# Kernel optimization log

Measured on AMD Instinct MI355X. Metric: run time of the kernel, lower is better.

The kernel has to match this reference:

```python
import jax, jax.numpy as jnp
import numpy as np

I, H, L, O = 11, 33, 3, 18

def lstm_layer(x_tbi, W_ih, W_hh, b_ih, b_hh):
    # x_tbi: [T, B, in]; W_ih: [4H, in]; W_hh: [4H, H]
    T, B = x_tbi.shape[0], x_tbi.shape[1]
    # precompute input contribution for all timesteps (one big GEMM)
    xg = jnp.einsum('tbi,gi->tbg', x_tbi, W_ih) + b_ih + b_hh  # [T, B, 4H]
    h0 = jnp.zeros((B, H), x_tbi.dtype)
    c0 = jnp.zeros((B, H), x_tbi.dtype)

    def step(carry, xg_t):
        h, c = carry
        gates = xg_t + h @ W_hh.T                      # [B, 4H]
        i, f, g, o = jnp.split(gates, 4, axis=-1)      # PyTorch gate order i,f,g,o
        i = jax.nn.sigmoid(i)
        f = jax.nn.sigmoid(f)
        g = jnp.tanh(g)
        o = jax.nn.sigmoid(o)
        c = f * c + i * g
        h = o * jnp.tanh(c)
        return (h, c), h

    (hT, cT), ys = jax.lax.scan(step, (h0, c0), xg)
    return ys, hT, cT  # ys: [T, B, H]


def setup_inputs() -> dict:
    key = jax.random.key(0)
    ks = jax.random.split(key, 20)
    B, T = 512, 2048
    s = 1.0 / np.sqrt(H)
    d = {'x': jax.random.normal(ks[0], (B, T, I), jnp.float32)}
    in_sizes = [I, H, H]
    for l in range(L):
        d[f'W_ih{l}'] = jax.random.uniform(ks[1 + 4 * l], (4 * H, in_sizes[l]), jnp.float32, -s, s)
        d[f'W_hh{l}'] = jax.random.uniform(ks[2 + 4 * l], (4 * H, H), jnp.float32, -s, s)
        d[f'b_ih{l}'] = jax.random.uniform(ks[3 + 4 * l], (4 * H,), jnp.float32, -s, s)
        d[f'b_hh{l}'] = jax.random.uniform(ks[4 + 4 * l], (4 * H,), jnp.float32, -s, s)
    d['W1'] = jax.random.normal(ks[13], (4 * O, H), jnp.float32) * 0.05
    d['b1'] = jnp.zeros((4 * O,), jnp.float32)
    d['W2'] = jax.random.normal(ks[14], (O, 4 * O), jnp.float32) * 0.05
    d['b2'] = jnp.zeros((O,), jnp.float32)
    return d


def reference(x, W_ih0, W_hh0, b_ih0, b_hh0, W_ih1, W_hh1, b_ih1, b_hh1,
              W_ih2, W_hh2, b_ih2, b_hh2, W1, b1, W2, b2):
    # x: [B, T, I] (batch_first) -> time-major for scan
    xt = jnp.transpose(x, (1, 0, 2))  # [T, B, I]
    params = [(W_ih0, W_hh0, b_ih0, b_hh0),
              (W_ih1, W_hh1, b_ih1, b_hh1),
              (W_ih2, W_hh2, b_ih2, b_hh2)]
    hiddens = []
    cur = xt
    for (Wi, Wh, bi, bh) in params:
        cur, hT, _ = lstm_layer(cur, Wi, Wh, bi, bh)
        hiddens.append(hT)
    hidden = jnp.stack(hiddens, axis=0)  # [L, B, H] (final hidden state per layer)
    # MLP head (dropout inactive at inference); torch nn.GELU default = exact erf
    h1 = jax.nn.gelu(hidden @ W1.T + b1, approximate=False)
    out = h1 @ W2.T + b2  # [L, B, O]
    return out, hidden
```

## Files before the change

kernel.cpp:

```cpp
#include <hip/hip_runtime.h>
#include <math.h>

#define TT 2048
#define BB 512
#define II 11
#define HH 33
#define NL 3
#define OO 18
#define HSLOT 48

typedef _Float16 h2 __attribute__((ext_vector_type(2)));
typedef _Float16 h8 __attribute__((ext_vector_type(8)));

__device__ __forceinline__ float sigm_f(float x) {
    float e = __expf(-x);
    return __builtin_amdgcn_rcpf(1.0f + e);
}
__device__ __forceinline__ float tanh_f(float x) {
    float e = __expf(2.0f * x);
    return 1.0f - 2.0f * __builtin_amdgcn_rcpf(e + 1.0f);
}

__device__ __forceinline__ h8 gldh8(const float* p, int k0, int rem) {
    h8 v;
    #pragma unroll
    for (int i = 0; i < 8; ++i) v[i] = (_Float16)((k0 + i < rem) ? p[k0 + i] : 0.0f);
    return v;
}
__device__ __forceinline__ h2 gldh2(const float* p, int k0, int rem) {
    h2 v;
    v.x = (_Float16)((k0 + 0 < rem) ? p[k0 + 0] : 0.0f);
    v.y = (_Float16)((k0 + 1 < rem) ? p[k0 + 1] : 0.0f);
    return v;
}

#define D8(a, v, w) do { \
    a = __builtin_amdgcn_fdot2((v).s01, (w).s01, a, false); \
    a = __builtin_amdgcn_fdot2((v).s23, (w).s23, a, false); \
    a = __builtin_amdgcn_fdot2((v).s45, (w).s45, a, false); \
    a = __builtin_amdgcn_fdot2((v).s67, (w).s67, a, false); } while (0)
#define D1(a, v, w) a = __builtin_amdgcn_fdot2((v), (w), a, false)

__global__ __launch_bounds__(128, 1) void lstm_pipeline_kernel(
    const float* __restrict__ x,
    const float* __restrict__ Wih0, const float* __restrict__ Whh0,
    const float* __restrict__ bih0, const float* __restrict__ bhh0,
    const float* __restrict__ Wih1, const float* __restrict__ Whh1,
    const float* __restrict__ bih1, const float* __restrict__ bhh1,
    const float* __restrict__ Wih2, const float* __restrict__ Whh2,
    const float* __restrict__ bih2, const float* __restrict__ bhh2,
    float* __restrict__ hidden_out)
{
    __shared__ __align__(16) _Float16 buf[2][NL + 1][HSLOT];

    const int tid = threadIdx.x;
    const int bg  = blockIdx.x;

    for (int i = tid; i < 2 * (NL + 1) * HSLOT; i += 128)
        ((_Float16*)buf)[i] = (_Float16)0.0f;

    const bool comp = (tid < 99);
    const int  u    = tid;
    const int  l    = (u < 33) ? 0 : (u < 66) ? 1 : 2;
    const int  j    = u - 33 * l;

    const int  pi   = tid - 99;
    const bool pref = (pi >= 0) && (pi < II);
    const float* xrow = x + (size_t)bg * TT * II + (pref ? pi : 0);

    h8 z8 = {0,0,0,0,0,0,0,0};
    h2 z2 = {(_Float16)0.0f, (_Float16)0.0f};
    h8 x00=z8,x01=z8,x02=z8,x03=z8; h2 x0t=z2;
    h8 x10=z8,x11=z8,x12=z8,x13=z8; h2 x1t=z2;
    h8 x20=z8,x21=z8,x22=z8,x23=z8; h2 x2t=z2;
    h8 x30=z8,x31=z8,x32=z8,x33=z8; h2 x3t=z2;
    h8 h00=z8,h01=z8,h02=z8,h03=z8; h2 h0t=z2;
    h8 h10=z8,h11=z8,h12=z8,h13=z8; h2 h1t=z2;
    h8 h20=z8,h21=z8,h22=z8,h23=z8; h2 h2t=z2;
    h8 h30=z8,h31=z8,h32=z8,h33=z8; h2 h3t=z2;
    float b0 = 0.0f, b1 = 0.0f, b2 = 0.0f, b3 = 0.0f;

    if (comp) {
        const float* bip = (l == 0) ? bih0 : (l == 1) ? bih1 : bih2;
        const float* bhp = (l == 0) ? bhh0 : (l == 1) ? bhh1 : bhh2;
        b0 = bip[0 * HH + j] + bhp[0 * HH + j];
        b1 = bip[1 * HH + j] + bhp[1 * HH + j];
        b2 = bip[2 * HH + j] + bhp[2 * HH + j];
        b3 = bip[3 * HH + j] + bhp[3 * HH + j];

        const float* Wi = (l == 0) ? Wih0 : (l == 1) ? Wih1 : Wih2;
        const float* Wh = (l == 0) ? Whh0 : (l == 1) ? Whh1 : Whh2;
        const int kin = (l == 0) ? II : HH;
        const float* r0 = Wi + (0 * HH + j) * kin;
        const float* r1 = Wi + (1 * HH + j) * kin;
        const float* r2 = Wi + (2 * HH + j) * kin;
        const float* r3 = Wi + (3 * HH + j) * kin;
        x00=gldh8(r0,0,kin); x01=gldh8(r0,8,kin); x02=gldh8(r0,16,kin); x03=gldh8(r0,24,kin); x0t=gldh2(r0,32,kin);
        x10=gldh8(r1,0,kin); x11=gldh8(r1,8,kin); x12=gldh8(r1,16,kin); x13=gldh8(r1,24,kin); x1t=gldh2(r1,32,kin);
        x20=gldh8(r2,0,kin); x21=gldh8(r2,8,kin); x22=gldh8(r2,16,kin); x23=gldh8(r2,24,kin); x2t=gldh2(r2,32,kin);
        x30=gldh8(r3,0,kin); x31=gldh8(r3,8,kin); x32=gldh8(r3,16,kin); x33=gldh8(r3,24,kin); x3t=gldh2(r3,32,kin);
        const float* s0 = Wh + (0 * HH + j) * HH;
        const float* s1 = Wh + (1 * HH + j) * HH;
        const float* s2 = Wh + (2 * HH + j) * HH;
        const float* s3 = Wh + (3 * HH + j) * HH;
        h00=gldh8(s0,0,HH); h01=gldh8(s0,8,HH); h02=gldh8(s0,16,HH); h03=gldh8(s0,24,HH); h0t=gldh2(s0,32,HH);
        h10=gldh8(s1,0,HH); h11=gldh8(s1,8,HH); h12=gldh8(s1,16,HH); h13=gldh8(s1,24,HH); h1t=gldh2(s1,32,HH);
        h20=gldh8(s2,0,HH); h21=gldh8(s2,8,HH); h22=gldh8(s2,16,HH); h23=gldh8(s2,24,HH); h2t=gldh2(s2,32,HH);
        h30=gldh8(s3,0,HH); h31=gldh8(s3,8,HH); h32=gldh8(s3,16,HH); h33=gldh8(s3,24,HH); h3t=gldh2(s3,32,HH);
    }

    __syncthreads();
    float v_next = 0.0f, v_next2 = 0.0f;
    if (pref) {
        buf[0][0][pi] = (_Float16)xrow[0];
        v_next  = xrow[II];
        v_next2 = xrow[2 * II];
    }
    __syncthreads();

    float c = 0.0f;

    const _Float16* rin[2]  = { &buf[0][l][0],     &buf[1][l][0] };
    const _Float16* rown[2] = { &buf[0][l + 1][0], &buf[1][l + 1][0] };
    _Float16*       wrp[2]  = { &buf[0][l + 1][j], &buf[1][l + 1][j] };
    _Float16*       pxp[2]  = { &buf[0][0][pi],    &buf[1][0][pi] };

    auto step = [&](int s, int rp, bool check, bool out, bool xload, bool xstore)
        __attribute__((always_inline)) {
        const int wp = rp ^ 1;
        if (pref) {
            if (xstore) *pxp[wp] = (_Float16)v_next;
            v_next = v_next2;
            if (xload) v_next2 = xrow[(size_t)(s + 3) * II];
        }
        const bool active = check ? (comp && (s >= l) && (s - l < TT)) : comp;
        if (active) {
            const h8* VI = (const h8*)rin[rp];
            const h8 vi0 = VI[0], vi1 = VI[1], vi2 = VI[2], vi3 = VI[3];
            const h2 vit = *(const h2*)(rin[rp] + 32);
            const h8* VO = (const h8*)rown[rp];
            const h8 vo0 = VO[0], vo1 = VO[1], vo2 = VO[2], vo3 = VO[3];
            const h2 vot = *(const h2*)(rown[rp] + 32);

            float a0 = b0, a1 = b1, a2 = b2, a3 = b3;
            D8(a0, vi0, x00); D8(a1, vi0, x10); D8(a2, vi0, x20); D8(a3, vi0, x30);
            D8(a0, vi1, x01); D8(a1, vi1, x11); D8(a2, vi1, x21); D8(a3, vi1, x31);
            D8(a0, vi2, x02); D8(a1, vi2, x12); D8(a2, vi2, x22); D8(a3, vi2, x32);
            D8(a0, vi3, x03); D8(a1, vi3, x13); D8(a2, vi3, x23); D8(a3, vi3, x33);
            D1(a0, vit, x0t); D1(a1, vit, x1t); D1(a2, vit, x2t); D1(a3, vit, x3t);
            D8(a0, vo0, h00); D8(a1, vo0, h10); D8(a2, vo0, h20); D8(a3, vo0, h30);
            D8(a0, vo1, h01); D8(a1, vo1, h11); D8(a2, vo1, h21); D8(a3, vo1, h31);
            D8(a0, vo2, h02); D8(a1, vo2, h12); D8(a2, vo2, h22); D8(a3, vo2, h32);
            D8(a0, vo3, h03); D8(a1, vo3, h13); D8(a2, vo3, h23); D8(a3, vo3, h33);
            D1(a0, vot, h0t); D1(a1, vot, h1t); D1(a2, vot, h2t); D1(a3, vot, h3t);

            const float ig = sigm_f(a0);
            const float fg = sigm_f(a1);
            const float gg = tanh_f(a2);
            const float og = sigm_f(a3);
            c = __builtin_fmaf(fg, c, ig * gg);
            const float hnew = og * tanh_f(c);

            *wrp[wp] = (_Float16)hnew;
            if (out && (s - l == TT - 1))
                hidden_out[((size_t)l * BB + bg) * HH + j] = hnew;
        }
        __syncthreads();
    };

    step(0, 0, true, false, true, true);
    step(1, 1, true, false, true, true);
    for (int s = 2; s < TT - 4; s += 2) {
        step(s,     0, false, false, true, true);
        step(s + 1, 1, false, false, true, true);
    }
    step(TT - 4, 0, false, false, true,  true);
    step(TT - 3, 1, false, false, false, true);
    step(TT - 2, 0, false, false, false, true);
    step(TT - 1, 1, false, true,  false, false);
    step(TT,     0, true,  true,  false, false);
    step(TT + 1, 1, true,  true,  false, false);
}

__global__ void mlp_head_kernel(const float* __restrict__ hidden,
                                const float* __restrict__ W1, const float* __restrict__ b1,
                                const float* __restrict__ W2, const float* __restrict__ b2,
                                float* __restrict__ out)
{
    const int row = blockIdx.x * blockDim.x + threadIdx.x;
    if (row >= NL * BB) return;

    float hv[HH];
    #pragma unroll
    for (int k = 0; k < HH; ++k) hv[k] = hidden[row * HH + k];

    float h1[4 * OO];
    #pragma unroll
    for (int m = 0; m < 4 * OO; ++m) {
        float a = b1[m];
        #pragma unroll
        for (int k = 0; k < HH; ++k) a += hv[k] * W1[m * HH + k];
        h1[m] = 0.5f * a * (1.0f + erff(a * 0.70710678118654752f));
    }
    #pragma unroll
    for (int o = 0; o < OO; ++o) {
        float a = b2[o];
        #pragma unroll
        for (int m = 0; m < 4 * OO; ++m) a += h1[m] * W2[o * (4 * OO) + m];
        out[row * OO + o] = a;
    }
}

extern "C" void kernel_launch(void* const* d_in, const int* in_sizes, int n_in,
                              void* d_out, int out_size, void* d_ws, size_t ws_size,
                              hipStream_t stream) {
    const float* x    = (const float*)d_in[0];
    const float* Wih0 = (const float*)d_in[1];
    const float* Whh0 = (const float*)d_in[2];
    const float* bih0 = (const float*)d_in[3];
    const float* bhh0 = (const float*)d_in[4];
    const float* Wih1 = (const float*)d_in[5];
    const float* Whh1 = (const float*)d_in[6];
    const float* bih1 = (const float*)d_in[7];
    const float* bhh1 = (const float*)d_in[8];
    const float* Wih2 = (const float*)d_in[9];
    const float* Whh2 = (const float*)d_in[10];
    const float* bih2 = (const float*)d_in[11];
    const float* bhh2 = (const float*)d_in[12];
    const float* W1   = (const float*)d_in[13];
    const float* b1   = (const float*)d_in[14];
    const float* W2   = (const float*)d_in[15];
    const float* b2   = (const float*)d_in[16];

    float* out    = (float*)d_out;
    float* hidden = out + NL * BB * OO;

    lstm_pipeline_kernel<<<BB, 128, 0, stream>>>(
        x, Wih0, Whh0, bih0, bhh0, Wih1, Whh1, bih1, bhh1,
        Wih2, Whh2, bih2, bhh2, hidden);

    mlp_head_kernel<<<(NL * BB + 255) / 256, 256, 0, stream>>>(
        hidden, W1, b1, W2, b2, out);
}
```

Before: 1.150 ms.

## Fuse MLP head into LSTM kernel and split gate dot products into two phases

Each block now computes the MLP head for its own batch row from final hidden states kept in shared memory, so the second kernel launch and the hidden-state round trip through global memory go away. The per-step gate computation is also reordered so the input and forget gates are finished and sent through sigmoid before the cell and output gate dot products start, letting transcendental latency overlap with FMA work. The cost is extra shared memory and a small serial tail at the end of each block.

```diff
diff --git a/kernel.cpp b/kernel.cpp
--- a/kernel.cpp
+++ b/kernel.cpp
@@ -49,9 +49,14 @@
     const float* __restrict__ bih1, const float* __restrict__ bhh1,
     const float* __restrict__ Wih2, const float* __restrict__ Whh2,
     const float* __restrict__ bih2, const float* __restrict__ bhh2,
-    float* __restrict__ hidden_out)
+    const float* __restrict__ W1, const float* __restrict__ b1,
+    const float* __restrict__ W2, const float* __restrict__ b2,
+    float* __restrict__ hidden_out,
+    float* __restrict__ outp)
 {
     __shared__ __align__(16) _Float16 buf[2][NL + 1][HSLOT];
+    __shared__ float hfin[NL][HH + 1];
+    __shared__ float h1s[NL][4 * OO];
 
     const int tid = threadIdx.x;
     const int bg  = blockIdx.x;
@@ -78,15 +83,15 @@
     h8 h10=z8,h11=z8,h12=z8,h13=z8; h2 h1t=z2;
     h8 h20=z8,h21=z8,h22=z8,h23=z8; h2 h2t=z2;
     h8 h30=z8,h31=z8,h32=z8,h33=z8; h2 h3t=z2;
-    float b0 = 0.0f, b1 = 0.0f, b2 = 0.0f, b3 = 0.0f;
+    float b0 = 0.0f, b1v = 0.0f, b2v = 0.0f, b3v = 0.0f;
 
     if (comp) {
         const float* bip = (l == 0) ? bih0 : (l == 1) ? bih1 : bih2;
         const float* bhp = (l == 0) ? bhh0 : (l == 1) ? bhh1 : bhh2;
-        b0 = bip[0 * HH + j] + bhp[0 * HH + j];
-        b1 = bip[1 * HH + j] + bhp[1 * HH + j];
-        b2 = bip[2 * HH + j] + bhp[2 * HH + j];
-        b3 = bip[3 * HH + j] + bhp[3 * HH + j];
+        b0  = bip[0 * HH + j] + bhp[0 * HH + j];
+        b1v = bip[1 * HH + j] + bhp[1 * HH + j];
+        b2v = bip[2 * HH + j] + bhp[2 * HH + j];
+        b3v = bip[3 * HH + j] + bhp[3 * HH + j];
 
         const float* Wi = (l == 0) ? Wih0 : (l == 1) ? Wih1 : Wih2;
         const float* Wh = (l == 0) ? Whh0 : (l == 1) ? Whh1 : Whh2;
@@ -142,28 +147,42 @@
             const h8 vo0 = VO[0], vo1 = VO[1], vo2 = VO[2], vo3 = VO[3];
             const h2 vot = *(const h2*)(rown[rp] + 32);
 
-            float a0 = b0, a1 = b1, a2 = b2, a3 = b3;
-            D8(a0, vi0, x00); D8(a1, vi0, x10); D8(a2, vi0, x20); D8(a3, vi0, x30);
-            D8(a0, vi1, x01); D8(a1, vi1, x11); D8(a2, vi1, x21); D8(a3, vi1, x31);
-            D8(a0, vi2, x02); D8(a1, vi2, x12); D8(a2, vi2, x22); D8(a3, vi2, x32);
-            D8(a0, vi3, x03); D8(a1, vi3, x13); D8(a2, vi3, x23); D8(a3, vi3, x33);
-            D1(a0, vit, x0t); D1(a1, vit, x1t); D1(a2, vit, x2t); D1(a3, vit, x3t);
-            D8(a0, vo0, h00); D8(a1, vo0, h10); D8(a2, vo0, h20); D8(a3, vo0, h30);
-            D8(a0, vo1, h01); D8(a1, vo1, h11); D8(a2, vo1, h21); D8(a3, vo1, h31);
-            D8(a0, vo2, h02); D8(a1, vo2, h12); D8(a2, vo2, h22); D8(a3, vo2, h32);
-            D8(a0, vo3, h03); D8(a1, vo3, h13); D8(a2, vo3, h23); D8(a3, vo3, h33);
-            D1(a0, vot, h0t); D1(a1, vot, h1t); D1(a2, vot, h2t); D1(a3, vot, h3t);
-
+            float a0 = b0, a1 = b1v;
+            D8(a1, vi0, x10); D8(a0, vi0, x00);
+            D8(a1, vi1, x11); D8(a0, vi1, x01);
+            D8(a1, vi2, x12); D8(a0, vi2, x02);
+            D8(a1, vi3, x13); D8(a0, vi3, x03);
+            D1(a1, vit, x1t); D1(a0, vit, x0t);
+            D8(a1, vo0, h10); D8(a0, vo0, h00);
+            D8(a1, vo1, h11); D8(a0, vo1, h01);
+            D8(a1, vo2, h12); D8(a0, vo2, h02);
+            D8(a1, vo3, h13); D8(a0, vo3, h03);
+            D1(a1, vot, h1t); D1(a0, vot, h0t);
+            const float fg = sigm_f(a1);
             const float ig = sigm_f(a0);
-            const float fg = sigm_f(a1);
+
+            float a2 = b2v, a3 = b3v;
+            D8(a2, vi0, x20); D8(a3, vi0, x30);
+            D8(a2, vi1, x21); D8(a3, vi1, x31);
+            D8(a2, vi2, x22); D8(a3, vi2, x32);
+            D8(a2, vi3, x23); D8(a3, vi3, x33);
+            D1(a2, vit, x2t); D1(a3, vit, x3t);
+            D8(a2, vo0, h20); D8(a3, vo0, h30);
+            D8(a2, vo1, h21); D8(a3, vo1, h31);
+            D8(a2, vo2, h22); D8(a3, vo2, h32);
+            D8(a2, vo3, h23); D8(a3, vo3, h33);
+            D1(a2, vot, h2t); D1(a3, vot, h3t);
+
             const float gg = tanh_f(a2);
             const float og = sigm_f(a3);
             c = __builtin_fmaf(fg, c, ig * gg);
             const float hnew = og * tanh_f(c);
 
             *wrp[wp] = (_Float16)hnew;
-            if (out && (s - l == TT - 1))
+            if (out && (s - l == TT - 1)) {
                 hidden_out[((size_t)l * BB + bg) * HH + j] = hnew;
+                hfin[l][j] = hnew;
+            }
         }
         __syncthreads();
     };
@@ -180,34 +199,23 @@
     step(TT - 1, 1, false, true,  false, false);
     step(TT,     0, true,  true,  false, false);
     step(TT + 1, 1, true,  true,  false, false);
-}
-
-__global__ void mlp_head_kernel(const float* __restrict__ hidden,
-                                const float* __restrict__ W1, const float* __restrict__ b1,
-                                const float* __restrict__ W2, const float* __restrict__ b2,
-                                float* __restrict__ out)
-{
-    const int row = blockIdx.x * blockDim.x + threadIdx.x;
-    if (row >= NL * BB) return;
-
-    float hv[HH];
-    #pragma unroll
-    for (int k = 0; k < HH; ++k) hv[k] = hidden[row * HH + k];
-
-    float h1[4 * OO];
-    #pragma unroll
-    for (int m = 0; m < 4 * OO; ++m) {
-        float a = b1[m];
+
+    if (tid < 4 * OO) {
         #pragma unroll
-        for (int k = 0; k < HH; ++k) a += hv[k] * W1[m * HH + k];
-        h1[m] = 0.5f * a * (1.0f + erff(a * 0.70710678118654752f));
-    }
-    #pragma unroll
-    for (int o = 0; o < OO; ++o) {
+        for (int ml = 0; ml < NL; ++ml) {
+            float a = b1[tid];
+            #pragma unroll
+            for (int k = 0; k < HH; ++k) a += hfin[ml][k] * W1[tid * HH + k];
+            h1s[ml][tid] = 0.5f * a * (1.0f + erff(a * 0.70710678118654752f));
+        }
+    }
+    __syncthreads();
+    if (tid < NL * OO) {
+        const int ol = tid / OO, o = tid % OO;
         float a = b2[o];
         #pragma unroll
-        for (int m = 0; m < 4 * OO; ++m) a += h1[m] * W2[o * (4 * OO) + m];
-        out[row * OO + o] = a;
+        for (int m = 0; m < 4 * OO; ++m) a += h1s[ol][m] * W2[o * (4 * OO) + m];
+        outp[((size_t)ol * BB + bg) * OO + o] = a;
     }
 }
 
@@ -237,8 +245,5 @@
 
     lstm_pipeline_kernel<<<BB, 128, 0, stream>>>(
         x, Wih0, Whh0, bih0, bhh0, Wih1, Whh1, bih1, bhh1,
-        Wih2, Whh2, bih2, bhh2, hidden);
-
-    mlp_head_kernel<<<(NL * BB + 255) / 256, 256, 0, stream>>>(
-        hidden, W1, b1, W2, b2, out);
-}
+        Wih2, Whh2, bih2, bhh2, W1, b1, W2, b2, hidden, out);
+}
```

After: 1.050 ms. 8.7% less time.
